# Optimization experiments

Hardware: AMD Instinct MI355X
Metric: run time of the kernel (lower is better)

Reference implementation:

```python
import jax, jax.numpy as jnp
import numpy as np

DIM_IN = 1024
DIM_OUT = 1024
BATCH = 4
SEQ = 2048


def setup_inputs() -> dict:
    key = jax.random.key(0)
    kx, kq, kk, kv = jax.random.split(key, 4)
    scale = 1.0 / np.sqrt(DIM_IN)
    x = jax.random.normal(kx, (BATCH, SEQ, DIM_IN), dtype=jnp.float32)
    # Weights stored as [dim_in, dim_out] (transpose of torch Linear's [out, in]);
    # y = x @ W is equivalent math to torch's x @ W_t.T
    Wq = jax.random.normal(kq, (DIM_IN, DIM_OUT), dtype=jnp.float32) * scale
    Wk = jax.random.normal(kk, (DIM_IN, DIM_OUT), dtype=jnp.float32) * scale
    Wv = jax.random.normal(kv, (DIM_IN, DIM_OUT), dtype=jnp.float32) * scale
    return {"x": x, "Wq": Wq, "Wk": Wk, "Wv": Wv}


def reference(x, Wq, Wk, Wv):
    # x: [b, s, d_in]; single-head causal self-attention (dropout=0 -> identity)
    q = jnp.einsum("bsd,de->bse", x, Wq)
    k = jnp.einsum("bsd,de->bse", x, Wk)
    v = jnp.einsum("bsd,de->bse", x, Wv)
    dim_k = k.shape[-1]
    scores = jnp.einsum("bqe,bke->bqk", q, k) / jnp.sqrt(jnp.float32(dim_k))
    s = x.shape[1]
    causal = jnp.tril(jnp.ones((s, s), dtype=bool))  # True = keep
    scores = jnp.where(causal[None, :, :], scores, -jnp.inf)
    weights = jax.nn.softmax(scores, axis=-1)
    context = jnp.einsum("bqk,bke->bqe", weights, v)
    return context
```

## Files before the change

kernel.cpp:

```cpp
#include <hip/hip_runtime.h>
#include <cstdint>
#include <cstddef>

typedef unsigned short u16;
typedef __bf16 bf16x8 __attribute__((ext_vector_type(8)));
typedef float f32x4 __attribute__((ext_vector_type(4)));

__device__ inline u16 f2b(float f) {
    uint32_t u = __builtin_bit_cast(uint32_t, f);
    u += 0x7FFFu + ((u >> 16) & 1u);
    return (u16)(u >> 16);
}

__device__ inline void gl2lds16(const u16* g, u16* l) {
    __builtin_amdgcn_global_load_lds(
        (const __attribute__((address_space(1))) void*)g,
        (__attribute__((address_space(3))) void*)l, 16, 0, 0);
}

__global__ void convert_x_kernel(const float* __restrict__ x, u16* __restrict__ xb) {
    size_t i = ((size_t)blockIdx.x * 256 + threadIdx.x) * 4;
    float4 v = *(const float4*)(x + i);
    uint2 pack;
    pack.x = (uint32_t)f2b(v.x) | ((uint32_t)f2b(v.y) << 16);
    pack.y = (uint32_t)f2b(v.z) | ((uint32_t)f2b(v.w) << 16);
    *(uint2*)(xb + i) = pack;
}

__global__ void transpose_w_kernel(const float* __restrict__ Wq,
                                   const float* __restrict__ Wk,
                                   const float* __restrict__ Wv,
                                   u16* __restrict__ QKWT, u16* __restrict__ WvT) {
    __shared__ u16 t[32][33];
    const int z = blockIdx.z;
    const float* W = (z == 0) ? Wq : ((z == 1) ? Wk : Wv);
    u16* dst = (z == 0) ? QKWT : ((z == 1) ? QKWT + 1024 * 1024 : WvT);
    const float scale = (z == 0) ? 0.03125f : 1.0f;
    const int bx = blockIdx.x * 32;
    const int by = blockIdx.y * 32;
    const int tx = threadIdx.x, ty = threadIdx.y;
    #pragma unroll
    for (int r = 0; r < 32; r += 8)
        t[ty + r][tx] = f2b(W[(size_t)(by + ty + r) * 1024 + bx + tx] * scale);
    __syncthreads();
    #pragma unroll
    for (int r = 0; r < 32; r += 8)
        dst[(size_t)(bx + ty + r) * 1024 + (by + tx)] = t[tx][ty + r];
}

template<int EPI>
__device__ __forceinline__ void gemm_body(
    u16* __restrict__ smem,
    const u16* __restrict__ A, int lda,
    const u16* __restrict__ B, int ldb,
    char* __restrict__ Cb, int ldc,
    int m0, int n0, int Kloc, float* __restrict__ lrow) {
    constexpr int BK = 32;
    const int tid = threadIdx.x;
    const int lane = tid & 63, wave = tid >> 6;
    const int wm = wave >> 1, wn = wave & 1;
    const int fl = lane & 15, fh = lane >> 4;

    const int q0 = wave * 2;
    const int srow = lane >> 2, skoff = (lane & 3) * 8;
    const u16* ApL0 = A + (size_t)(m0 + q0 * 16 + srow) * lda + skoff;
    const u16* ApL1 = ApL0 + (size_t)16 * lda;
    const u16* BpL0 = B + (size_t)(n0 + q0 * 16 + srow) * ldb + skoff;
    const u16* BpL1 = BpL0 + (size_t)16 * ldb;

    u16* const Ab[2] = { smem, smem + 4096 };
    u16* const Bb[2] = { smem + 8192, smem + 12288 };

    auto issue = [&](int buf, int k0) {
        gl2lds16(ApL0 + k0, Ab[buf] + q0 * 512);
        gl2lds16(ApL1 + k0, Ab[buf] + q0 * 512 + 512);
        gl2lds16(BpL0 + k0, Bb[buf] + q0 * 512);
        gl2lds16(BpL1 + k0, Bb[buf] + q0 * 512 + 512);
    };

    const f32x4 vzero = {0.f, 0.f, 0.f, 0.f};
    f32x4 acc[4][4];
    #pragma unroll
    for (int i = 0; i < 4; ++i)
        #pragma unroll
        for (int j = 0; j < 4; ++j) acc[i][j] = vzero;

    issue(0, 0);
    int buf = 0;
    for (int k0 = 0; k0 < Kloc; k0 += BK, buf ^= 1) {
        __syncthreads();
        if (k0 + BK < Kloc) issue(buf ^ 1, k0 + BK);
        bf16x8 af[4], bfr[4];
        #pragma unroll
        for (int t = 0; t < 4; ++t) {
            af[t]  = *(const bf16x8*)&Ab[buf][(wm * 64 + t * 16 + fl) * BK + fh * 8];
            bfr[t] = *(const bf16x8*)&Bb[buf][(wn * 64 + t * 16 + fl) * BK + fh * 8];
        }
        #pragma unroll
        for (int mt = 0; mt < 4; ++mt)
            #pragma unroll
            for (int nt = 0; nt < 4; ++nt)
                acc[mt][nt] = __builtin_amdgcn_mfma_f32_16x16x32_bf16(
                    af[mt], bfr[nt], acc[mt][nt], 0, 0, 0);
    }

    if (EPI == 0) {
        u16* Cp = (u16*)Cb;
        #pragma unroll
        for (int mt = 0; mt < 4; ++mt)
            #pragma unroll
            for (int nt = 0; nt < 4; ++nt)
                #pragma unroll
                for (int r = 0; r < 4; ++r) {
                    int row = m0 + wm * 64 + mt * 16 + fh * 4 + r;
                    int col = n0 + wn * 64 + nt * 16 + fl;
                    Cp[(size_t)row * ldc + col] = f2b(acc[mt][nt][r]);
                }
    } else if (EPI == 2) {
        u16* Cp = (u16*)Cb;
        #pragma unroll
        for (int mt = 0; mt < 4; ++mt)
            #pragma unroll
            for (int r = 0; r < 4; ++r) {
                int row = m0 + wm * 64 + mt * 16 + fh * 4 + r;
                float part = 0.f;
                #pragma unroll
                for (int nt = 0; nt < 4; ++nt) {
                    int col = n0 + wn * 64 + nt * 16 + fl;
                    float p = (col <= row) ? __expf(acc[mt][nt][r]) : 0.f;
                    part += p;
                    Cp[(size_t)row * ldc + col] = f2b(p);
                }
                #pragma unroll
                for (int off = 1; off < 16; off <<= 1)
                    part += __shfl_xor(part, off, 64);
                if (fl == 0) atomicAdd(lrow + row, part);
            }
    } else {
        float* Cp = (float*)Cb;
        #pragma unroll
        for (int mt = 0; mt < 4; ++mt)
            #pragma unroll
            for (int r = 0; r < 4; ++r) {
                int row = m0 + wm * 64 + mt * 16 + fh * 4 + r;
                float inv = 1.0f / lrow[row];
                #pragma unroll
                for (int nt = 0; nt < 4; ++nt) {
                    int col = n0 + wn * 64 + nt * 16 + fl;
                    Cp[(size_t)row * ldc + col] = acc[mt][nt][r] * inv;
                }
            }
    }
}

__global__ __launch_bounds__(256)
void proj_kernel(const u16* __restrict__ xb, const u16* __restrict__ QKWT,
                 const u16* __restrict__ WvT, u16* __restrict__ QK,
                 u16* __restrict__ Vt) {
    __shared__ __align__(16) u16 smem[16384];
    int bid = blockIdx.x;
    const u16 *A, *B;
    char* C;
    int lda, ldb, ldc, m0, n0;
    if (bid < 1024) {
        int jt = bid & 15, it = bid >> 4;
        A = xb;  lda = 1024;  B = QKWT;  ldb = 1024;
        C = (char*)QK;  ldc = 2048;  m0 = it * 128;  n0 = jt * 128;
    } else {
        int b = bid - 1024;
        int jt = b & 63, it = b >> 6;
        A = WvT;  lda = 1024;  B = xb;  ldb = 1024;
        C = (char*)Vt;  ldc = 8192;  m0 = it * 128;  n0 = jt * 128;
    }
    gemm_body<0>(smem, A, lda, B, ldb, C, ldc, m0, n0, 1024, nullptr);
}

__global__ __launch_bounds__(256)
void scores_kernel(const u16* __restrict__ QK, u16* __restrict__ P,
                   float* __restrict__ l) {
    __shared__ __align__(16) u16 smem[16384];
    const int t = blockIdx.x, z = blockIdx.y;
    int it = (int)((sqrtf(8.0f * t + 1.0f) - 1.0f) * 0.5f);
    while ((it + 1) * (it + 2) / 2 <= t) ++it;
    while (it * (it + 1) / 2 > t) --it;
    const int jt = t - it * (it + 1) / 2;
    const u16* Qz = QK + (size_t)z * 2048 * 2048;
    const u16* Kz = Qz + 1024;
    u16* Pz = P + (size_t)z * 2048 * 2048;
    gemm_body<2>(smem, Qz, 2048, Kz, 2048, (char*)Pz, 2048,
                 it * 128, jt * 128, 1024, l + (size_t)z * 2048);
}

__global__ __launch_bounds__(256)
void out_kernel(const u16* __restrict__ P, const u16* __restrict__ Vt,
                float* __restrict__ out, float* __restrict__ l) {
    __shared__ __align__(16) u16 smem[16384];
    const int jt = blockIdx.x;
    const int it = 15 - (int)blockIdx.y;
    const int z = blockIdx.z;
    gemm_body<3>(smem, P + (size_t)z * 2048 * 2048, 2048,
                 Vt + (size_t)z * 2048, 8192,
                 (char*)(out + (size_t)z * 2048 * 1024), 1024,
                 it * 128, jt * 128, (it + 1) * 128, l + (size_t)z * 2048);
}

extern "C" void kernel_launch(void* const* d_in, const int* in_sizes, int n_in,
                              void* d_out, int out_size, void* d_ws, size_t ws_size,
                              hipStream_t stream) {
    (void)in_sizes; (void)n_in; (void)out_size; (void)ws_size;
    const float* x  = (const float*)d_in[0];
    const float* Wq = (const float*)d_in[1];
    const float* Wk = (const float*)d_in[2];
    const float* Wv = (const float*)d_in[3];
    float* out = (float*)d_out;

    const size_t MB = 1u << 20;
    char* ws = (char*)d_ws;
    u16* xb   = (u16*)(ws);
    u16* QKWT = (u16*)(ws + 16 * MB);
    u16* WvT  = (u16*)(ws + 20 * MB);
    u16* QK   = (u16*)(ws + 22 * MB);
    u16* Vt   = (u16*)(ws + 54 * MB);
    u16* P    = (u16*)(ws + 70 * MB);
    float* l  = (float*)(ws + 102 * MB);

    hipMemsetAsync(l, 0, 8192 * sizeof(float), stream);
    convert_x_kernel<<<8192, 256, 0, stream>>>(x, xb);
    transpose_w_kernel<<<dim3(32, 32, 3), dim3(32, 8), 0, stream>>>(Wq, Wk, Wv, QKWT, WvT);

    proj_kernel<<<1536, 256, 0, stream>>>(xb, QKWT, WvT, QK, Vt);
    scores_kernel<<<dim3(136, 4), 256, 0, stream>>>(QK, P, l);
    out_kernel<<<dim3(8, 16, 4), 256, 0, stream>>>(P, Vt, out, l);
}
```

Measured before the change: 265.5 us.

## Enlarge GEMM tiles to 256x256 with 512 threads and 4-stage LDS pipeline

```diff
diff --git a/kernel.cpp b/kernel.cpp
--- a/kernel.cpp
+++ b/kernel.cpp
@@ -16,6 +16,10 @@
     __builtin_amdgcn_global_load_lds(
         (const __attribute__((address_space(1))) void*)g,
         (__attribute__((address_space(3))) void*)l, 16, 0, 0);
+}
+
+template<int N> __device__ __forceinline__ void waitvm() {
+    asm volatile("s_waitcnt vmcnt(%0)" :: "n"(N) : "memory");
 }
 
 __global__ void convert_x_kernel(const float* __restrict__ x, u16* __restrict__ xb) {
@@ -48,85 +52,111 @@
         dst[(size_t)(bx + ty + r) * 1024 + (by + tx)] = t[tx][ty + r];
 }
 
-template<int EPI>
-__device__ __forceinline__ void gemm_body(
+template<int NFRAG, int EPI>
+__device__ __forceinline__ void gemm256(
     u16* __restrict__ smem,
     const u16* __restrict__ A, int lda,
     const u16* __restrict__ B, int ldb,
     char* __restrict__ Cb, int ldc,
     int m0, int n0, int Kloc, float* __restrict__ lrow) {
-    constexpr int BK = 32;
-    const int tid = threadIdx.x;
+    constexpr int BK  = 32;
+    constexpr int ASZ = 256 * BK;
+    constexpr int BSZ = NFRAG * 64 * BK;
+    constexpr int LPT = 2 + NFRAG / 2;
+
+    const int tid  = threadIdx.x;
     const int lane = tid & 63, wave = tid >> 6;
-    const int wm = wave >> 1, wn = wave & 1;
+    const int wm = wave >> 2, wn = wave & 3;
     const int fl = lane & 15, fh = lane >> 4;
 
-    const int q0 = wave * 2;
-    const int srow = lane >> 2, skoff = (lane & 3) * 8;
-    const u16* ApL0 = A + (size_t)(m0 + q0 * 16 + srow) * lda + skoff;
-    const u16* ApL1 = ApL0 + (size_t)16 * lda;
-    const u16* BpL0 = B + (size_t)(n0 + q0 * 16 + srow) * ldb + skoff;
-    const u16* BpL1 = BpL0 + (size_t)16 * ldb;
-
-    u16* const Ab[2] = { smem, smem + 4096 };
-    u16* const Bb[2] = { smem + 8192, smem + 12288 };
-
-    auto issue = [&](int buf, int k0) {
-        gl2lds16(ApL0 + k0, Ab[buf] + q0 * 512);
-        gl2lds16(ApL1 + k0, Ab[buf] + q0 * 512 + 512);
-        gl2lds16(BpL0 + k0, Bb[buf] + q0 * 512);
-        gl2lds16(BpL1 + k0, Bb[buf] + q0 * 512 + 512);
+    const int r0 = tid >> 2;
+    const int ko = (tid & 3) * 8;
+    const u16* Ap0 = A + (size_t)(m0 + r0) * lda + ko;
+    const u16* Ap1 = Ap0 + (size_t)128 * lda;
+    const u16* Bp0 = B + (size_t)(n0 + r0) * ldb + ko;
+    const u16* Bp1 = Bp0 + (size_t)128 * ldb;
+
+    u16* const Ab = smem;
+    u16* const Bb = smem + 4 * ASZ;
+
+    auto stage = [&](int t) {
+        const int buf = t & 3;
+        const int k0  = t * BK;
+        u16* Ad = Ab + buf * ASZ + wave * 512;
+        gl2lds16(Ap0 + k0, Ad);
+        gl2lds16(Ap1 + k0, Ad + 4096);
+        u16* Bd = Bb + buf * BSZ + wave * 512;
+        gl2lds16(Bp0 + k0, Bd);
+        if constexpr (NFRAG == 4) gl2lds16(Bp1 + k0, Bd + 4096);
     };
 
     const f32x4 vzero = {0.f, 0.f, 0.f, 0.f};
-    f32x4 acc[4][4];
+    f32x4 acc[8][NFRAG];
     #pragma unroll
-    for (int i = 0; i < 4; ++i)
-        #pragma unroll
-        for (int j = 0; j < 4; ++j) acc[i][j] = vzero;
-
-    issue(0, 0);
-    int buf = 0;
-    for (int k0 = 0; k0 < Kloc; k0 += BK, buf ^= 1) {
-        __syncthreads();
-        if (k0 + BK < Kloc) issue(buf ^ 1, k0 + BK);
-        bf16x8 af[4], bfr[4];
-        #pragma unroll
-        for (int t = 0; t < 4; ++t) {
-            af[t]  = *(const bf16x8*)&Ab[buf][(wm * 64 + t * 16 + fl) * BK + fh * 8];
-            bfr[t] = *(const bf16x8*)&Bb[buf][(wn * 64 + t * 16 + fl) * BK + fh * 8];
-        }
-        #pragma unroll
-        for (int mt = 0; mt < 4; ++mt)
-            #pragma unroll
-            for (int nt = 0; nt < 4; ++nt)
+    for (int i = 0; i < 8; ++i)
+        #pragma unroll
+        for (int j = 0; j < NFRAG; ++j) acc[i][j] = vzero;
+
+    const int NT = Kloc >> 5;
+    stage(0); stage(1); stage(2);
+
+    for (int t = 0; t < NT; ++t) {
+        if (t + 3 < NT) stage(t + 3);
+        const int nafter = (NT - 1 - t) < 3 ? (NT - 1 - t) : 3;
+        if (nafter == 3)      waitvm<3 * LPT>();
+        else if (nafter == 2) waitvm<2 * LPT>();
+        else if (nafter == 1) waitvm<LPT>();
+        else                  waitvm<0>();
+        __builtin_amdgcn_s_barrier();
+        asm volatile("" ::: "memory");
+
+        const u16* At = Ab + (t & 3) * ASZ;
+        const u16* Bt = Bb + (t & 3) * BSZ;
+        bf16x8 af[8], bfr[NFRAG];
+        #pragma unroll
+        for (int mt = 0; mt < 8; ++mt)
+            af[mt] = *(const bf16x8*)&At[(wm * 128 + mt * 16 + fl) * BK + fh * 8];
+        #pragma unroll
+        for (int nt = 0; nt < NFRAG; ++nt)
+            bfr[nt] = *(const bf16x8*)&Bt[(wn * (NFRAG * 16) + nt * 16 + fl) * BK + fh * 8];
+
+        __builtin_amdgcn_s_setprio(1);
+        #pragma unroll
+        for (int mt = 0; mt < 8; ++mt)
+            #pragma unroll
+            for (int nt = 0; nt < NFRAG; ++nt)
                 acc[mt][nt] = __builtin_amdgcn_mfma_f32_16x16x32_bf16(
                     af[mt], bfr[nt], acc[mt][nt], 0, 0, 0);
+        __builtin_amdgcn_s_setprio(0);
+
+        asm volatile("s_waitcnt lgkmcnt(0)" ::: "memory");
+        __builtin_amdgcn_s_barrier();
+        asm volatile("" ::: "memory");
     }
 
-    if (EPI == 0) {
+    const int rbase = m0 + wm * 128 + fh * 4;
+    const int cbase = n0 + wn * (NFRAG * 16) + fl;
+    if constexpr (EPI == 0) {
         u16* Cp = (u16*)Cb;
         #pragma unroll
-        for (int mt = 0; mt < 4; ++mt)
-            #pragma unroll
-            for (int nt = 0; nt < 4; ++nt)
-                #pragma unroll
-                for (int r = 0; r < 4; ++r) {
-                    int row = m0 + wm * 64 + mt * 16 + fh * 4 + r;
-                    int col = n0 + wn * 64 + nt * 16 + fl;
-                    Cp[(size_t)row * ldc + col] = f2b(acc[mt][nt][r]);
-                }
-    } else if (EPI == 2) {
+        for (int mt = 0; mt < 8; ++mt)
+            #pragma unroll
+            for (int nt = 0; nt < NFRAG; ++nt)
+                #pragma unroll
+                for (int r = 0; r < 4; ++r)
+                    Cp[(size_t)(rbase + mt * 16 + r) * ldc + cbase + nt * 16] =
+                        f2b(acc[mt][nt][r]);
+    } else if constexpr (EPI == 2) {
         u16* Cp = (u16*)Cb;
         #pragma unroll
-        for (int mt = 0; mt < 4; ++mt)
+        for (int mt = 0; mt < 8; ++mt)
             #pragma unroll
             for (int r = 0; r < 4; ++r) {
-                int row = m0 + wm * 64 + mt * 16 + fh * 4 + r;
+                const int row = rbase + mt * 16 + r;
                 float part = 0.f;
                 #pragma unroll
-                for (int nt = 0; nt < 4; ++nt) {
-                    int col = n0 + wn * 64 + nt * 16 + fl;
+                for (int nt = 0; nt < NFRAG; ++nt) {
+                    const int col = cbase + nt * 16;
                     float p = (col <= row) ? __expf(acc[mt][nt][r]) : 0.f;
                     part += p;
                     Cp[(size_t)row * ldc + col] = f2b(p);
@@ -139,46 +169,44 @@
     } else {
         float* Cp = (float*)Cb;
         #pragma unroll
-        for (int mt = 0; mt < 4; ++mt)
+        for (int mt = 0; mt < 8; ++mt)
             #pragma unroll
             for (int r = 0; r < 4; ++r) {
-                int row = m0 + wm * 64 + mt * 16 + fh * 4 + r;
-                float inv = 1.0f / lrow[row];
-                #pragma unroll
-                for (int nt = 0; nt < 4; ++nt) {
-                    int col = n0 + wn * 64 + nt * 16 + fl;
-                    Cp[(size_t)row * ldc + col] = acc[mt][nt][r] * inv;
-                }
+                const int row = rbase + mt * 16 + r;
+                const float inv = 1.0f / lrow[row];
+                #pragma unroll
+                for (int nt = 0; nt < NFRAG; ++nt)
+                    Cp[(size_t)row * ldc + cbase + nt * 16] = acc[mt][nt][r] * inv;
             }
     }
 }
 
-__global__ __launch_bounds__(256)
+__global__ __launch_bounds__(512, 2)
 void proj_kernel(const u16* __restrict__ xb, const u16* __restrict__ QKWT,
                  const u16* __restrict__ WvT, u16* __restrict__ QK,
                  u16* __restrict__ Vt) {
-    __shared__ __align__(16) u16 smem[16384];
-    int bid = blockIdx.x;
+    __shared__ __align__(16) u16 smem[65536];
+    const int bid = blockIdx.x;
     const u16 *A, *B;
     char* C;
-    int lda, ldb, ldc, m0, n0;
-    if (bid < 1024) {
-        int jt = bid & 15, it = bid >> 4;
-        A = xb;  lda = 1024;  B = QKWT;  ldb = 1024;
-        C = (char*)QK;  ldc = 2048;  m0 = it * 128;  n0 = jt * 128;
+    int ldc, m0, n0;
+    if (bid < 256) {
+        const int it = bid >> 3, jt = bid & 7;
+        A = xb;  B = QKWT;  C = (char*)QK;  ldc = 2048;
+        m0 = it * 256;  n0 = jt * 256;
     } else {
-        int b = bid - 1024;
-        int jt = b & 63, it = b >> 6;
-        A = WvT;  lda = 1024;  B = xb;  ldb = 1024;
-        C = (char*)Vt;  ldc = 8192;  m0 = it * 128;  n0 = jt * 128;
+        const int b = bid - 256;
+        const int it = b >> 5, jt = b & 31;
+        A = WvT;  B = xb;  C = (char*)Vt;  ldc = 8192;
+        m0 = it * 256;  n0 = jt * 256;
     }
-    gemm_body<0>(smem, A, lda, B, ldb, C, ldc, m0, n0, 1024, nullptr);
-}
-
-__global__ __launch_bounds__(256)
+    gemm256<4, 0>(smem, A, 1024, B, 1024, C, ldc, m0, n0, 1024, nullptr);
+}
+
+__global__ __launch_bounds__(512, 2)
 void scores_kernel(const u16* __restrict__ QK, u16* __restrict__ P,
                    float* __restrict__ l) {
-    __shared__ __align__(16) u16 smem[16384];
+    __shared__ __align__(16) u16 smem[65536];
     const int t = blockIdx.x, z = blockIdx.y;
     int it = (int)((sqrtf(8.0f * t + 1.0f) - 1.0f) * 0.5f);
     while ((it + 1) * (it + 2) / 2 <= t) ++it;
@@ -187,21 +215,21 @@
     const u16* Qz = QK + (size_t)z * 2048 * 2048;
     const u16* Kz = Qz + 1024;
     u16* Pz = P + (size_t)z * 2048 * 2048;
-    gemm_body<2>(smem, Qz, 2048, Kz, 2048, (char*)Pz, 2048,
-                 it * 128, jt * 128, 1024, l + (size_t)z * 2048);
-}
-
-__global__ __launch_bounds__(256)
+    gemm256<4, 2>(smem, Qz, 2048, Kz, 2048, (char*)Pz, 2048,
+                  it * 256, jt * 256, 1024, l + (size_t)z * 2048);
+}
+
+__global__ __launch_bounds__(512, 2)
 void out_kernel(const u16* __restrict__ P, const u16* __restrict__ Vt,
                 float* __restrict__ out, float* __restrict__ l) {
-    __shared__ __align__(16) u16 smem[16384];
+    __shared__ __align__(16) u16 smem[49152];
     const int jt = blockIdx.x;
-    const int it = 15 - (int)blockIdx.y;
+    const int it = 7 - (int)blockIdx.y;
     const int z = blockIdx.z;
-    gemm_body<3>(smem, P + (size_t)z * 2048 * 2048, 2048,
-                 Vt + (size_t)z * 2048, 8192,
-                 (char*)(out + (size_t)z * 2048 * 1024), 1024,
-                 it * 128, jt * 128, (it + 1) * 128, l + (size_t)z * 2048);
+    gemm256<2, 3>(smem, P + (size_t)z * 2048 * 2048, 2048,
+                  Vt + (size_t)z * 2048, 8192,
+                  (char*)(out + (size_t)z * 2048 * 1024), 1024,
+                  it * 256, jt * 128, (it + 1) * 256, l + (size_t)z * 2048);
 }
 
 extern "C" void kernel_launch(void* const* d_in, const int* in_sizes, int n_in,
@@ -228,7 +256,7 @@
     convert_x_kernel<<<8192, 256, 0, stream>>>(x, xb);
     transpose_w_kernel<<<dim3(32, 32, 3), dim3(32, 8), 0, stream>>>(Wq, Wk, Wv, QKWT, WvT);
 
-    proj_kernel<<<1536, 256, 0, stream>>>(xb, QKWT, WvT, QK, Vt);
-    scores_kernel<<<dim3(136, 4), 256, 0, stream>>>(QK, P, l);
-    out_kernel<<<dim3(8, 16, 4), 256, 0, stream>>>(P, Vt, out, l);
-}
+    proj_kernel<<<384, 512, 0, stream>>>(xb, QKWT, WvT, QK, Vt);
+    scores_kernel<<<dim3(36, 4), 512, 0, stream>>>(QK, P, l);
+    out_kernel<<<dim3(8, 8, 4), 512, 0, stream>>>(P, Vt, out, l);
+}
```

Result: faster. 259.1 us (-2.4%).
